# Kernel optimization log

Hardware: AMD Instinct MI355X
Metric: run time of the kernel (lower is better)

## Reference

```python
import jax, jax.numpy as jnp
import numpy as np

THETA = 10000.0

def _rope(x, cos, sin):
    # x: [B, S, D]; cos/sin: [S, D/2]. Pairs are (x[..., 2i], x[..., 2i+1]) treated as complex.
    xr = x.reshape(*x.shape[:-1], -1, 2)
    x0, x1 = xr[..., 0], xr[..., 1]
    o0 = x0 * cos - x1 * sin
    o1 = x0 * sin + x1 * cos
    return jnp.stack([o0, o1], axis=-1).reshape(x.shape)

def setup_inputs() -> dict:
    key = jax.random.key(0)
    ks = jax.random.split(key, 7)
    B, S, D = 4, 2048, 1024
    sd = 1.0 / np.sqrt(D)
    return {
        "x": jax.random.normal(ks[0], (B, S, D), dtype=jnp.float32),
        "wq_w": jax.random.normal(ks[1], (D, D), dtype=jnp.float32) * sd,
        "wq_b": jax.random.normal(ks[2], (D,), dtype=jnp.float32) * 0.01,
        "wk_w": jax.random.normal(ks[3], (D, D), dtype=jnp.float32) * sd,
        "wk_b": jax.random.normal(ks[4], (D,), dtype=jnp.float32) * 0.01,
        "wv_w": jax.random.normal(ks[5], (D, D), dtype=jnp.float32) * sd,
        "wv_b": jax.random.normal(ks[6], (D,), dtype=jnp.float32) * 0.01,
    }

def reference(x, wq_w, wq_b, wk_w, wk_b, wv_w, wv_b):
    B, S, D = x.shape
    # QKV projections (torch Linear: y = x @ W.T + b)
    q = jnp.einsum('bsd,ed->bse', x, wq_w) + wq_b
    k = jnp.einsum('bsd,ed->bse', x, wk_w) + wk_b
    v = jnp.einsum('bsd,ed->bse', x, wv_w) + wv_b
    # Rotary embedding: freqs_cis[t, i] = exp(i * t / theta^(2i/D))
    inv_freq = 1.0 / (THETA ** (jnp.arange(0, D, 2, dtype=jnp.float32) / D))  # [D/2]
    ang = jnp.arange(S, dtype=jnp.float32)[:, None] * inv_freq[None, :]  # [S, D/2]
    cos, sin = jnp.cos(ang), jnp.sin(ang)
    q = _rope(q, cos, sin)
    k = _rope(k, cos, sin)
    # Full (non-causal, single-head) attention with scale 1/sqrt(dim)
    scores = jnp.einsum('bqd,bkd->bqk', q, k) / jnp.sqrt(jnp.float32(D))
    probs = jax.nn.softmax(scores.astype(jnp.float32), axis=-1)
    return jnp.einsum('bqk,bkd->bqd', probs, v)
```

## Files before the change

### kernel.cpp

```cpp
#include <hip/hip_runtime.h>
#include <cstdint>

using u16 = unsigned short;
using u32 = unsigned int;

typedef __attribute__((ext_vector_type(8))) short short8;
typedef __attribute__((ext_vector_type(4))) float floatx4;

__device__ __forceinline__ u16 f2bf(float f) {
    u32 u = __float_as_uint(f);
    u32 r = u + 0x7fffu + ((u >> 16) & 1u);
    return (u16)(r >> 16);
}
__device__ __forceinline__ float bf2f(u16 h) {
    return __uint_as_float(((u32)h) << 16);
}

__global__ void cvt_all(const float* __restrict__ x, u16* __restrict__ xb,
                        const float* __restrict__ w0, const float* __restrict__ w1,
                        const float* __restrict__ w2,
                        u16* __restrict__ o0, u16* __restrict__ o1, u16* __restrict__ o2,
                        const float* __restrict__ qb, const float* __restrict__ kb,
                        float* __restrict__ bqk, float* __restrict__ rowsum)
{
    int b = blockIdx.x;
    if (b >= 11272) {
        long i = ((long)(b - 11272) * 256 + threadIdx.x) * 4;
        *reinterpret_cast<float4*>(rowsum + i) = make_float4(0.f, 0.f, 0.f, 0.f);
        return;
    }
    if (b >= 11264) {
        int i = (b - 11264) * 256 + threadIdx.x;
        bqk[i] = (i < 1024) ? qb[i] : kb[i - 1024];
        return;
    }
    const float* src; u16* dst; long base;
    if (b < 8192) { src = x; dst = xb; base = (long)b; }
    else {
        int r = b - 8192, seg = r >> 10;
        if (seg == 0)      { src = w0; dst = o0; }
        else if (seg == 1) { src = w1; dst = o1; }
        else               { src = w2; dst = o2; }
        base = (long)(r & 1023);
    }
    long i = (base * 256 + threadIdx.x) * 4;
    float4 v = *reinterpret_cast<const float4*>(src + i);
    uint2 o;
    o.x = (u32)f2bf(v.x) | ((u32)f2bf(v.y) << 16);
    o.y = (u32)f2bf(v.z) | ((u32)f2bf(v.w) << 16);
    *reinterpret_cast<uint2*>(dst + i) = o;
}

__device__ __forceinline__ void async_cp16(const u16* g, u16* l) {
    __builtin_amdgcn_global_load_lds(
        (const __attribute__((address_space(1))) void*)g,
        (__attribute__((address_space(3))) void*)l, 16, 0, 0);
}

template <bool BF16_OUT, bool EXPOUT>
__device__ __forceinline__ void gemm_core(
    const u16* __restrict__ A, const u16* __restrict__ B, void* __restrict__ Cv,
    int K, int lda, int ldb, int ldc,
    long tile_m, long tile_n, long cbase,
    const float* bias_col, const float* bias_row,
    float scale, bool rope, float* __restrict__ rowsum, u16* smem)
{
    u16* As = smem;
    u16* Bs = smem + 8192;

    const int tid  = threadIdx.x;
    const int lane = tid & 63;
    const int wave = tid >> 6;
    const int wm = (wave >> 1) << 6;
    const int wn = (wave & 1) << 6;

    floatx4 acc[4][4] = {};

    const int srow = tid >> 2;
    const int skp  = (((tid & 3) ^ (srow & 3))) * 8;
    const u16* Ag = A + (tile_m + srow) * (long)lda + skp;
    const u16* Bg = B + (tile_n + srow) * (long)ldb + skp;
    u16* Asl = &As[tid * 8];
    u16* Bsl = &Bs[tid * 8];

    const int fm  = lane & 15;
    const int fks = (((lane >> 4) ^ (lane & 3))) * 8;

    for (int k0 = 0; k0 < K; k0 += 64) {
        async_cp16(Ag,                       Asl);
        async_cp16(Ag + 64 * (long)lda,      Asl + 64 * 32);
        async_cp16(Ag + 32,                  Asl + 4096);
        async_cp16(Ag + 32 + 64 * (long)lda, Asl + 4096 + 64 * 32);
        async_cp16(Bg,                       Bsl);
        async_cp16(Bg + 64 * (long)ldb,      Bsl + 64 * 32);
        async_cp16(Bg + 32,                  Bsl + 4096);
        async_cp16(Bg + 32 + 64 * (long)ldb, Bsl + 4096 + 64 * 32);
        Ag += 64; Bg += 64;
        __syncthreads();

        #pragma unroll
        for (int c = 0; c < 2; ++c) {
            const u16* Ap = As + c * 4096;
            const u16* Bp = Bs + c * 4096;
            short8 af[4], bfr[4];
            #pragma unroll
            for (int i = 0; i < 4; ++i)
                af[i] = *reinterpret_cast<const short8*>(&Ap[(wm + i * 16 + fm) * 32 + fks]);
            #pragma unroll
            for (int j = 0; j < 4; ++j)
                bfr[j] = *reinterpret_cast<const short8*>(&Bp[(wn + j * 16 + fm) * 32 + fks]);
            #pragma unroll
            for (int i = 0; i < 4; ++i)
                #pragma unroll
                for (int j = 0; j < 4; ++j)
                    acc[i][j] = __builtin_amdgcn_mfma_f32_16x16x32_bf16(af[i], bfr[j], acc[i][j], 0, 0, 0);
        }
        __syncthreads();
    }

    const int q4  = lane >> 4;
    const int c16 = lane & 15;
    float* smemf  = (float*)smem;
    float* myeps = smemf + wave * (16 * 68);
    const long n0 = tile_n + wn + c16 * 4;

    float4 bc4 = make_float4(0.f, 0.f, 0.f, 0.f);
    if (bias_col) bc4 = *reinterpret_cast<const float4*>(bias_col + n0);

    float inv0 = 0.f, inv1 = 0.f;
    if (rope) {
        int p0 = (int)(n0 >> 1);
        inv0 = __expf((float)(p0 & 511)       * -1.79889463e-2f);
        inv1 = __expf((float)((p0 + 1) & 511) * -1.79889463e-2f);
    }

    #pragma unroll
    for (int i = 0; i < 4; ++i) {
        #pragma unroll
        for (int j = 0; j < 4; ++j)
            #pragma unroll
            for (int r = 0; r < 4; ++r)
                myeps[(q4 * 4 + r) * 68 + j * 16 + c16] = acc[i][j][r];
        __syncthreads();
        #pragma unroll
        for (int p = 0; p < 4; ++p) {
            int lrow = p * 4 + q4;
            long m = tile_m + wm + i * 16 + lrow;
            float4 v = *reinterpret_cast<const float4*>(&myeps[lrow * 68 + c16 * 4]);
            v.x = v.x * scale + bc4.x;
            v.y = v.y * scale + bc4.y;
            v.z = v.z * scale + bc4.z;
            v.w = v.w * scale + bc4.w;
            if (bias_row) {
                float br = bias_row[m];
                v.x += br; v.y += br; v.z += br; v.w += br;
            }
            if (rope) {
                int s = (int)(m & 2047);
                float a0 = (float)s * inv0, a1 = (float)s * inv1;
                float sn0 = __sinf(a0), cs0 = __cosf(a0);
                float sn1 = __sinf(a1), cs1 = __cosf(a1);
                float x0 = v.x, x1 = v.y, x2 = v.z, x3 = v.w;
                v.x = x0 * cs0 - x1 * sn0;
                v.y = x0 * sn0 + x1 * cs0;
                v.z = x2 * cs1 - x3 * sn1;
                v.w = x2 * sn1 + x3 * cs1;
            }
            if constexpr (EXPOUT) {
                v.x = __expf(v.x); v.y = __expf(v.y);
                v.z = __expf(v.z); v.w = __expf(v.w);
                float s4 = v.x + v.y + v.z + v.w;
                s4 += __shfl_xor(s4, 1);
                s4 += __shfl_xor(s4, 2);
                s4 += __shfl_xor(s4, 4);
                s4 += __shfl_xor(s4, 8);
                if (c16 == 0) atomicAdd(&rowsum[m], s4);
            }
            long off = cbase + m * (long)ldc + n0;
            if constexpr (BF16_OUT) {
                uint2 o;
                o.x = (u32)f2bf(v.x) | ((u32)f2bf(v.y) << 16);
                o.y = (u32)f2bf(v.z) | ((u32)f2bf(v.w) << 16);
                *reinterpret_cast<uint2*>((u16*)Cv + off) = o;
            } else {
                *reinterpret_cast<float4*>((float*)Cv + off) = v;
            }
        }
        __syncthreads();
    }
}

template <bool BF16_OUT>
__device__ __forceinline__ void gemm_core_n64(
    const u16* __restrict__ A, const u16* __restrict__ B, void* __restrict__ Cv,
    int K, int lda, int ldb, int ldc,
    long tile_m, long tile_n, long cbase,
    float scale, const float* __restrict__ rowscale, u16* smem)
{
    u16* As = smem;
    u16* Bs = smem + 8192;

    const int tid  = threadIdx.x;
    const int lane = tid & 63;
    const int wave = tid >> 6;
    const int wm = (wave >> 1) << 6;
    const int wn = (wave & 1) << 5;

    floatx4 acc[4][2] = {};

    const int srow = tid >> 2;
    const int skp  = (((tid & 3) ^ (srow & 3))) * 8;
    const u16* Ag = A + (tile_m + srow) * (long)lda + skp;
    const u16* Bg = B + (tile_n + srow) * (long)ldb + skp;
    u16* Asl = &As[tid * 8];
    u16* Bsl = &Bs[tid * 8];

    const int fm  = lane & 15;
    const int fks = (((lane >> 4) ^ (lane & 3))) * 8;

    for (int k0 = 0; k0 < K; k0 += 64) {
        async_cp16(Ag,                       Asl);
        async_cp16(Ag + 64 * (long)lda,      Asl + 64 * 32);
        async_cp16(Ag + 32,                  Asl + 4096);
        async_cp16(Ag + 32 + 64 * (long)lda, Asl + 4096 + 64 * 32);
        async_cp16(Bg,                       Bsl);
        async_cp16(Bg + 32,                  Bsl + 2048);
        Ag += 64; Bg += 64;
        __syncthreads();

        #pragma unroll
        for (int c = 0; c < 2; ++c) {
            const u16* Ap = As + c * 4096;
            const u16* Bp = Bs + c * 2048;
            short8 af[4], bfr[2];
            #pragma unroll
            for (int i = 0; i < 4; ++i)
                af[i] = *reinterpret_cast<const short8*>(&Ap[(wm + i * 16 + fm) * 32 + fks]);
            #pragma unroll
            for (int j = 0; j < 2; ++j)
                bfr[j] = *reinterpret_cast<const short8*>(&Bp[(wn + j * 16 + fm) * 32 + fks]);
            #pragma unroll
            for (int i = 0; i < 4; ++i)
                #pragma unroll
                for (int j = 0; j < 2; ++j)
                    acc[i][j] = __builtin_amdgcn_mfma_f32_16x16x32_bf16(af[i], bfr[j], acc[i][j], 0, 0, 0);
        }
        __syncthreads();
    }

    const int q4  = lane >> 4;
    const int c16 = lane & 15;
    float* smemf = (float*)smem;
    float* myeps = smemf + wave * (16 * 36);
    const long n0 = tile_n + wn + c16 * 2;

    #pragma unroll
    for (int i = 0; i < 4; ++i) {
        #pragma unroll
        for (int j = 0; j < 2; ++j)
            #pragma unroll
            for (int r = 0; r < 4; ++r)
                myeps[(q4 * 4 + r) * 36 + j * 16 + c16] = acc[i][j][r];
        __syncthreads();
        #pragma unroll
        for (int p = 0; p < 4; ++p) {
            int lrow = p * 4 + q4;
            long m = tile_m + wm + i * 16 + lrow;
            float2 v = *reinterpret_cast<const float2*>(&myeps[lrow * 36 + c16 * 2]);
            float sc = scale;
            if (rowscale) sc *= 1.0f / rowscale[m];
            v.x *= sc; v.y *= sc;
            long off = cbase + m * (long)ldc + n0;
            if constexpr (BF16_OUT) {
                *reinterpret_cast<u32*>((u16*)Cv + off) =
                    (u32)f2bf(v.x) | ((u32)f2bf(v.y) << 16);
            } else {
                *reinterpret_cast<float2*>((float*)Cv + off) = v;
            }
        }
        __syncthreads();
    }
}

template <bool BF16_OUT, bool EXPOUT>
__global__ __launch_bounds__(256)
void gemm_nt(const u16* __restrict__ A, const u16* __restrict__ B, void* __restrict__ Cv,
             int K, int lda, int ldb, int ldc,
             long sA, long sB, long sC,
             const float* __restrict__ bias_col, const float* __restrict__ bias_row,
             float scale, float* __restrict__ rowsum)
{
    const u32 gx = gridDim.x, gy = gridDim.y;
    u32 id = blockIdx.x + gx * (blockIdx.y + gy * blockIdx.z);
    const u32 G = gx * gy * gridDim.z;
    if ((G & 7u) == 0u) id = (id & 7u) * (G >> 3) + (id >> 3);
    const u32 bx = id % gx;
    const u32 t1 = id / gx;
    const u32 by = t1 % gy;
    const u32 bz = t1 / gy;

    __shared__ alignas(16) u16 smem[16384];
    gemm_core<BF16_OUT, EXPOUT>(A + (long)bz * sA, B + (long)bz * sB, Cv,
                        K, lda, ldb, ldc,
                        (long)by * 128, (long)bx * 128, (long)bz * sC,
                        bias_col, bias_row, scale, false,
                        EXPOUT ? rowsum + (long)bz * 2048 : nullptr, smem);
}

template <bool BF16_OUT>
__global__ __launch_bounds__(256)
void gemm_nt_n64(const u16* __restrict__ A, const u16* __restrict__ B, void* __restrict__ Cv,
                 int K, int lda, int ldb, int ldc,
                 long sA, long sB, long sC, float scale,
                 const float* __restrict__ rowscale)
{
    const u32 gx = gridDim.x, gy = gridDim.y;
    u32 id = blockIdx.x + gx * (blockIdx.y + gy * blockIdx.z);
    const u32 G = gx * gy * gridDim.z;
    if ((G & 7u) == 0u) id = (id & 7u) * (G >> 3) + (id >> 3);
    const u32 bx = id % gx;
    const u32 t1 = id / gx;
    const u32 by = t1 % gy;
    const u32 bz = t1 / gy;

    __shared__ alignas(16) u16 smem[12288];
    gemm_core_n64<BF16_OUT>(A + (long)bz * sA, B + (long)bz * sB, Cv,
                            K, lda, ldb, ldc,
                            (long)by * 128, (long)bx * 64, (long)bz * sC,
                            scale, rowscale ? rowscale + (long)bz * 2048 : nullptr, smem);
}

__global__ __launch_bounds__(256)
void gemm_fused12(const u16* __restrict__ xb, const u16* __restrict__ wqk,
                  const u16* __restrict__ wv, u16* __restrict__ QK, u16* __restrict__ VT,
                  const float* __restrict__ bqk, const float* __restrict__ wvb)
{
    u32 id = blockIdx.x;
    id = (id & 7u) * 192u + (id >> 3);
    __shared__ alignas(16) u16 smem[16384];
    if (id < 1024u) {
        u32 bx = id & 15u, by = id >> 4;
        gemm_core<true, false>(xb, wqk, QK, 1024, 1024, 1024, 2048,
                        (long)by * 128, (long)bx * 128, 0L,
                        bqk, nullptr, 1.0f, true, nullptr, smem);
    } else {
        u32 r = id - 1024u;
        u32 bx = r & 15u, by = (r >> 4) & 7u, bz = r >> 7;
        gemm_core<true, false>(wv, xb + (long)bz * 2048 * 1024, VT,
                        1024, 1024, 1024, 2048,
                        (long)by * 128, (long)bx * 128, (long)bz * 1024 * 2048,
                        nullptr, wvb, 1.0f, false, nullptr, smem);
    }
}

extern "C" void kernel_launch(void* const* d_in, const int* in_sizes, int n_in,
                              void* d_out, int out_size, void* d_ws, size_t ws_size,
                              hipStream_t stream)
{
    const float* x   = (const float*)d_in[0];
    const float* wqw = (const float*)d_in[1];
    const float* wqb = (const float*)d_in[2];
    const float* wkw = (const float*)d_in[3];
    const float* wkb = (const float*)d_in[4];
    const float* wvw = (const float*)d_in[5];
    const float* wvb = (const float*)d_in[6];
    float* out = (float*)d_out;

    char* ws = (char*)d_ws;
    const size_t MB = 1ull << 20;
    u16*   Pbuf = (u16*)(ws + 64 * MB);
    u16*   QK   = (u16*)(ws + 96 * MB);
    u16*   VT   = (u16*)(ws + 128 * MB);
    float* rsum = (float*)(ws + 144 * MB);
    u16*   xb    = (u16*)(ws + 0);
    u16*   wqk   = (u16*)(ws + 16 * MB);
    u16*   wvbuf = (u16*)(ws + 20 * MB);
    float* bqk   = (float*)(ws + 22 * MB);

    cvt_all<<<dim3(11280), 256, 0, stream>>>(x, xb, wqw, wkw, wvw,
                                             wqk, wqk + 1024 * 1024, wvbuf,
                                             wqb, wkb, bqk, rsum);

    gemm_fused12<<<dim3(1536), 256, 0, stream>>>(xb, wqk, wvbuf, QK, VT, bqk, wvb);

    gemm_nt<true, true><<<dim3(16, 16, 4), 256, 0, stream>>>(
        QK, QK + 1024, Pbuf, 1024, 2048, 2048, 2048,
        2048L * 2048, 2048L * 2048, 2048L * 2048, nullptr, nullptr, 0.03125f, rsum);

    gemm_nt_n64<false><<<dim3(16, 16, 4), 256, 0, stream>>>(
        Pbuf, VT, out, 2048, 2048, 2048, 1024,
        2048L * 2048, 1024L * 2048, 2048L * 1024, 1.0f, rsum);

    (void)in_sizes; (void)n_in; (void)out_size; (void)ws_size;
}
```

Before: 263.4 us.

## Use 256x256 tiles with multi-stage async LDS pipeline for QKV and QK^T GEMMs

Replaces the 128x128, 256-thread GEMM core with a 256x256-tile, 512-thread core. It uses an 8-slot LDS ring buffer, explicit vmcnt waits and raw barriers, so that global-to-LDS copies for later k-steps overlap the current MFMA work. Scheduling barriers and setprio are added to keep the MFMA clusters contiguous. Both the fused QKV projection and the QK^T kernel switch to this core. The aim is more data reuse per tile and less load latency per k-step, at the cost of 128KB of LDS per block and fewer blocks in each grid (384 and 256), which risks imbalance across CUs.

Result: slower. 271.3 us (+3.0%).

```diff
diff --git a/kernel.cpp b/kernel.cpp
--- a/kernel.cpp
+++ b/kernel.cpp
@@ -11,9 +11,6 @@
     u32 u = __float_as_uint(f);
     u32 r = u + 0x7fffu + ((u >> 16) & 1u);
     return (u16)(r >> 16);
-}
-__device__ __forceinline__ float bf2f(u16 h) {
-    return __uint_as_float(((u32)h) << 16);
 }
 
 __global__ void cvt_all(const float* __restrict__ x, u16* __restrict__ xb,
@@ -57,72 +54,115 @@
         (__attribute__((address_space(3))) void*)l, 16, 0, 0);
 }
 
+#define MEMFENCE asm volatile("" ::: "memory")
+__device__ __forceinline__ void barrier_raw() {
+    MEMFENCE; __builtin_amdgcn_s_barrier(); MEMFENCE;
+}
+__device__ __forceinline__ void vmwait(int n) {
+    if      (n == 6) asm volatile("s_waitcnt vmcnt(6)" ::: "memory");
+    else if (n == 4) asm volatile("s_waitcnt vmcnt(4)" ::: "memory");
+    else if (n == 2) asm volatile("s_waitcnt vmcnt(2)" ::: "memory");
+    else             asm volatile("s_waitcnt vmcnt(0)" ::: "memory");
+}
+
 template <bool BF16_OUT, bool EXPOUT>
-__device__ __forceinline__ void gemm_core(
+__device__ __forceinline__ void gemm8_core(
     const u16* __restrict__ A, const u16* __restrict__ B, void* __restrict__ Cv,
     int K, int lda, int ldb, int ldc,
     long tile_m, long tile_n, long cbase,
-    const float* bias_col, const float* bias_row,
+    const float* __restrict__ bias_col, const float* __restrict__ bias_row,
     float scale, bool rope, float* __restrict__ rowsum, u16* smem)
 {
-    u16* As = smem;
-    u16* Bs = smem + 8192;
-
     const int tid  = threadIdx.x;
     const int lane = tid & 63;
     const int wave = tid >> 6;
-    const int wm = (wave >> 1) << 6;
-    const int wn = (wave & 1) << 6;
-
-    floatx4 acc[4][4] = {};
+    const int wm2  = (wave >> 2) * 128;
+    const int wn2  = (wave & 3) * 64;
+    const int fm   = lane & 15;
+    const int fks  = ((lane >> 4) ^ (lane & 3)) * 8;
 
     const int srow = tid >> 2;
-    const int skp  = (((tid & 3) ^ (srow & 3))) * 8;
-    const u16* Ag = A + (tile_m + srow) * (long)lda + skp;
-    const u16* Bg = B + (tile_n + srow) * (long)ldb + skp;
-    u16* Asl = &As[tid * 8];
-    u16* Bsl = &Bs[tid * 8];
-
-    const int fm  = lane & 15;
-    const int fks = (((lane >> 4) ^ (lane & 3))) * 8;
-
-    for (int k0 = 0; k0 < K; k0 += 64) {
-        async_cp16(Ag,                       Asl);
-        async_cp16(Ag + 64 * (long)lda,      Asl + 64 * 32);
-        async_cp16(Ag + 32,                  Asl + 4096);
-        async_cp16(Ag + 32 + 64 * (long)lda, Asl + 4096 + 64 * 32);
-        async_cp16(Bg,                       Bsl);
-        async_cp16(Bg + 64 * (long)ldb,      Bsl + 64 * 32);
-        async_cp16(Bg + 32,                  Bsl + 4096);
-        async_cp16(Bg + 32 + 64 * (long)ldb, Bsl + 4096 + 64 * 32);
-        Ag += 64; Bg += 64;
-        __syncthreads();
-
-        #pragma unroll
-        for (int c = 0; c < 2; ++c) {
-            const u16* Ap = As + c * 4096;
-            const u16* Bp = Bs + c * 4096;
-            short8 af[4], bfr[4];
-            #pragma unroll
-            for (int i = 0; i < 4; ++i)
-                af[i] = *reinterpret_cast<const short8*>(&Ap[(wm + i * 16 + fm) * 32 + fks]);
+    const int kgl  = ((tid & 3) ^ (srow & 3)) * 8;
+    const u16* Asrc = A + (tile_m + srow) * (long)lda + kgl;
+    const u16* Bsrc = B + (tile_n + srow) * (long)ldb + kgl;
+    u16* dst0 = smem + tid * 8;
+
+    const int U = K >> 5;
+
+    floatx4 acc[8][4] = {};
+    short8 bf[4];
+
+    auto stageA = [&](int v) {
+        u16* d = dst0 + ((2 * v) & 7) * 8192;
+        const u16* s = Asrc + v * 32;
+        async_cp16(s, d);
+        async_cp16(s + 128 * (long)lda, d + 4096);
+    };
+    auto stageB = [&](int v) {
+        u16* d = dst0 + ((2 * v + 1) & 7) * 8192;
+        const u16* s = Bsrc + v * 32;
+        async_cp16(s, d);
+        async_cp16(s + 128 * (long)ldb, d + 4096);
+    };
+
+    auto phase_pair = [&](int u, int vmx, int vmy, bool stb, bool sta)
+        __attribute__((always_inline))
+    {
+        const u16* Ap = smem + ((2 * u) & 7) * 8192;
+        const u16* Bp = smem + ((2 * u + 1) & 7) * 8192;
+        short8 af[4];
+        #pragma unroll
+        for (int i = 0; i < 4; ++i)
+            af[i] = *reinterpret_cast<const short8*>(&Ap[(wm2 + i * 16 + fm) * 32 + fks]);
+        #pragma unroll
+        for (int j = 0; j < 4; ++j)
+            bf[j] = *reinterpret_cast<const short8*>(&Bp[(wn2 + j * 16 + fm) * 32 + fks]);
+        if (stb) stageB(u + 2);
+        vmwait(vmx);
+        barrier_raw();
+        __builtin_amdgcn_sched_barrier(0);
+        __builtin_amdgcn_s_setprio(1);
+        #pragma unroll
+        for (int i = 0; i < 4; ++i)
             #pragma unroll
             for (int j = 0; j < 4; ++j)
-                bfr[j] = *reinterpret_cast<const short8*>(&Bp[(wn + j * 16 + fm) * 32 + fks]);
-            #pragma unroll
-            for (int i = 0; i < 4; ++i)
-                #pragma unroll
-                for (int j = 0; j < 4; ++j)
-                    acc[i][j] = __builtin_amdgcn_mfma_f32_16x16x32_bf16(af[i], bfr[j], acc[i][j], 0, 0, 0);
-        }
-        __syncthreads();
-    }
+                acc[i][j] = __builtin_amdgcn_mfma_f32_16x16x32_bf16(af[i], bf[j], acc[i][j], 0, 0, 0);
+        __builtin_amdgcn_s_setprio(0);
+        __builtin_amdgcn_sched_barrier(0);
+        barrier_raw();
+        #pragma unroll
+        for (int i = 0; i < 4; ++i)
+            af[i] = *reinterpret_cast<const short8*>(&Ap[(wm2 + 64 + i * 16 + fm) * 32 + fks]);
+        if (sta) stageA(u + 3);
+        vmwait(vmy);
+        barrier_raw();
+        __builtin_amdgcn_sched_barrier(0);
+        __builtin_amdgcn_s_setprio(1);
+        #pragma unroll
+        for (int i = 0; i < 4; ++i)
+            #pragma unroll
+            for (int j = 0; j < 4; ++j)
+                acc[4 + i][j] = __builtin_amdgcn_mfma_f32_16x16x32_bf16(af[i], bf[j], acc[4 + i][j], 0, 0, 0);
+        __builtin_amdgcn_s_setprio(0);
+        __builtin_amdgcn_sched_barrier(0);
+        barrier_raw();
+    };
+
+    stageA(0); stageB(0); stageA(1); stageB(1); stageA(2);
+    vmwait(6);
+    barrier_raw();
+
+    for (int u = 0; u + 3 < U; ++u)
+        phase_pair(u, 6, 6, true, true);
+    phase_pair(U - 3, 6, 4, true,  false);
+    phase_pair(U - 2, 2, 0, false, false);
+    phase_pair(U - 1, 0, 0, false, false);
 
     const int q4  = lane >> 4;
     const int c16 = lane & 15;
     float* smemf  = (float*)smem;
-    float* myeps = smemf + wave * (16 * 68);
-    const long n0 = tile_n + wn + c16 * 4;
+    float* myeps  = smemf + wave * (16 * 68);
+    const long n0 = tile_n + wn2 + c16 * 4;
 
     float4 bc4 = make_float4(0.f, 0.f, 0.f, 0.f);
     if (bias_col) bc4 = *reinterpret_cast<const float4*>(bias_col + n0);
@@ -135,7 +175,7 @@
     }
 
     #pragma unroll
-    for (int i = 0; i < 4; ++i) {
+    for (int i = 0; i < 8; ++i) {
         #pragma unroll
         for (int j = 0; j < 4; ++j)
             #pragma unroll
@@ -145,7 +185,7 @@
         #pragma unroll
         for (int p = 0; p < 4; ++p) {
             int lrow = p * 4 + q4;
-            long m = tile_m + wm + i * 16 + lrow;
+            long m = tile_m + wm2 + i * 16 + lrow;
             float4 v = *reinterpret_cast<const float4*>(&myeps[lrow * 68 + c16 * 4]);
             v.x = v.x * scale + bc4.x;
             v.y = v.y * scale + bc4.y;
@@ -190,6 +230,44 @@
     }
 }
 
+__global__ __launch_bounds__(512, 2)
+void gemm8_fused12(const u16* __restrict__ xb, const u16* __restrict__ wqk,
+                   const u16* __restrict__ wv, u16* __restrict__ QK, u16* __restrict__ VT,
+                   const float* __restrict__ bqk, const float* __restrict__ wvb)
+{
+    u32 id = blockIdx.x;
+    id = (id & 7u) * 48u + (id >> 3);
+    __shared__ alignas(16) u16 smem[65536];
+    if (id < 256u) {
+        u32 bx = id & 7u, by = id >> 3;
+        gemm8_core<true, false>(xb, wqk, QK, 1024, 1024, 1024, 2048,
+                                (long)by * 256, (long)bx * 256, 0L,
+                                bqk, nullptr, 1.0f, true, nullptr, smem);
+    } else {
+        u32 r = id - 256u;
+        u32 bz = r >> 5, q = r & 31u, bx = q & 7u, by = q >> 3;
+        gemm8_core<true, false>(wv, xb + (long)bz * 2048 * 1024, VT,
+                                1024, 1024, 1024, 2048,
+                                (long)by * 256, (long)bx * 256, (long)bz * 1024 * 2048,
+                                nullptr, wvb, 1.0f, false, nullptr, smem);
+    }
+}
+
+__global__ __launch_bounds__(512, 2)
+void gemm8_qkt(const u16* __restrict__ QK, u16* __restrict__ Pbuf,
+               float* __restrict__ rsum)
+{
+    u32 id = blockIdx.x;
+    id = (id & 7u) * 32u + (id >> 3);
+    u32 bz = id >> 6, q = id & 63u, bx = q & 7u, by = q >> 3;
+    __shared__ alignas(16) u16 smem[65536];
+    const u16* base = QK + (long)bz * 2048 * 2048;
+    gemm8_core<true, true>(base, base + 1024, Pbuf, 1024, 2048, 2048, 2048,
+                           (long)by * 256, (long)bx * 256, (long)bz * 2048 * 2048,
+                           nullptr, nullptr, 0.03125f, false,
+                           rsum + (long)bz * 2048, smem);
+}
+
 template <bool BF16_OUT>
 __device__ __forceinline__ void gemm_core_n64(
     const u16* __restrict__ A, const u16* __restrict__ B, void* __restrict__ Cv,
@@ -282,13 +360,12 @@
     }
 }
 
-template <bool BF16_OUT, bool EXPOUT>
+template <bool BF16_OUT>
 __global__ __launch_bounds__(256)
-void gemm_nt(const u16* __restrict__ A, const u16* __restrict__ B, void* __restrict__ Cv,
-             int K, int lda, int ldb, int ldc,
-             long sA, long sB, long sC,
-             const float* __restrict__ bias_col, const float* __restrict__ bias_row,
-             float scale, float* __restrict__ rowsum)
+void gemm_nt_n64(const u16* __restrict__ A, const u16* __restrict__ B, void* __restrict__ Cv,
+                 int K, int lda, int ldb, int ldc,
+                 long sA, long sB, long sC, float scale,
+                 const float* __restrict__ rowscale)
 {
     const u32 gx = gridDim.x, gy = gridDim.y;
     u32 id = blockIdx.x + gx * (blockIdx.y + gy * blockIdx.z);
@@ -299,58 +376,11 @@
     const u32 by = t1 % gy;
     const u32 bz = t1 / gy;
 
-    __shared__ alignas(16) u16 smem[16384];
-    gemm_core<BF16_OUT, EXPOUT>(A + (long)bz * sA, B + (long)bz * sB, Cv,
-                        K, lda, ldb, ldc,
-                        (long)by * 128, (long)bx * 128, (long)bz * sC,
-                        bias_col, bias_row, scale, false,
-                        EXPOUT ? rowsum + (long)bz * 2048 : nullptr, smem);
-}
-
-template <bool BF16_OUT>
-__global__ __launch_bounds__(256)
-void gemm_nt_n64(const u16* __restrict__ A, const u16* __restrict__ B, void* __restrict__ Cv,
-                 int K, int lda, int ldb, int ldc,
-                 long sA, long sB, long sC, float scale,
-                 const float* __restrict__ rowscale)
-{
-    const u32 gx = gridDim.x, gy = gridDim.y;
-    u32 id = blockIdx.x + gx * (blockIdx.y + gy * blockIdx.z);
-    const u32 G = gx * gy * gridDim.z;
-    if ((G & 7u) == 0u) id = (id & 7u) * (G >> 3) + (id >> 3);
-    const u32 bx = id % gx;
-    const u32 t1 = id / gx;
-    const u32 by = t1 % gy;
-    const u32 bz = t1 / gy;
-
     __shared__ alignas(16) u16 smem[12288];
     gemm_core_n64<BF16_OUT>(A + (long)bz * sA, B + (long)bz * sB, Cv,
                             K, lda, ldb, ldc,
                             (long)by * 128, (long)bx * 64, (long)bz * sC,
                             scale, rowscale ? rowscale + (long)bz * 2048 : nullptr, smem);
-}
-
-__global__ __launch_bounds__(256)
-void gemm_fused12(const u16* __restrict__ xb, const u16* __restrict__ wqk,
-                  const u16* __restrict__ wv, u16* __restrict__ QK, u16* __restrict__ VT,
-                  const float* __restrict__ bqk, const float* __restrict__ wvb)
-{
-    u32 id = blockIdx.x;
-    id = (id & 7u) * 192u + (id >> 3);
-    __shared__ alignas(16) u16 smem[16384];
-    if (id < 1024u) {
-        u32 bx = id & 15u, by = id >> 4;
-        gemm_core<true, false>(xb, wqk, QK, 1024, 1024, 1024, 2048,
-                        (long)by * 128, (long)bx * 128, 0L,
-                        bqk, nullptr, 1.0f, true, nullptr, smem);
-    } else {
-        u32 r = id - 1024u;
-        u32 bx = r & 15u, by = (r >> 4) & 7u, bz = r >> 7;
-        gemm_core<true, false>(wv, xb + (long)bz * 2048 * 1024, VT,
-                        1024, 1024, 1024, 2048,
-                        (long)by * 128, (long)bx * 128, (long)bz * 1024 * 2048,
-                        nullptr, wvb, 1.0f, false, nullptr, smem);
-    }
 }
 
 extern "C" void kernel_launch(void* const* d_in, const int* in_sizes, int n_in,
@@ -381,11 +411,9 @@
                                              wqk, wqk + 1024 * 1024, wvbuf,
                                              wqb, wkb, bqk, rsum);
 
-    gemm_fused12<<<dim3(1536), 256, 0, stream>>>(xb, wqk, wvbuf, QK, VT, bqk, wvb);
-
-    gemm_nt<true, true><<<dim3(16, 16, 4), 256, 0, stream>>>(
-        QK, QK + 1024, Pbuf, 1024, 2048, 2048, 2048,
-        2048L * 2048, 2048L * 2048, 2048L * 2048, nullptr, nullptr, 0.03125f, rsum);
+    gemm8_fused12<<<dim3(384), 512, 0, stream>>>(xb, wqk, wvbuf, QK, VT, bqk, wvb);
+
+    gemm8_qkt<<<dim3(256), 512, 0, stream>>>(QK, Pbuf, rsum);
 
     gemm_nt_n64<false><<<dim3(16, 16, 4), 256, 0, stream>>>(
         Pbuf, VT, out, 2048, 2048, 2048, 1024,
```
